# Kernel optimization log

Measured on AMD Instinct MI355X. Metric: run time of the kernel, lower is better.

Reference implementation:

```python
import jax, jax.numpy as jnp
import numpy as np

TOP_K = 2
EPS = 0.1
NUM_TOKENS = 524288
NUM_EXPERTS = 64
NEG_INF = -jnp.inf


def setup_inputs() -> dict:
    key = jax.random.key(0)
    router_logits = jax.random.normal(key, (NUM_TOKENS, NUM_EXPERTS), dtype=jnp.float32)
    return {"router_logits": router_logits}


def reference(router_logits):
    logits = router_logits.astype(jnp.float32)
    n = logits.shape[0]
    rows = jnp.arange(n)
    idx_list = []
    val_list = []
    for i in range(TOP_K):
        if i > 0:
            # mask out the previous maximum (argmax of current logits)
            prev = jnp.argmax(logits, axis=-1)
            logits = logits.at[rows, prev].set(NEG_INF)
        max_values = jnp.max(logits, axis=-1, keepdims=True)      # [n,1]
        max_indices = jnp.argmax(logits, axis=-1)                 # [n]
        # sparse-mixer mask: entries too far below the max get -inf
        denom = jnp.maximum(jnp.abs(logits), max_values)
        mask = (max_values - logits) / denom > 2.0 * EPS          # NaN at -inf entries -> False, kept -inf by logits value
        masked_logits = jnp.where(mask, NEG_INF, logits)
        sm = jax.nn.softmax(masked_logits, axis=-1)
        sel = jnp.take_along_axis(sm, max_indices[:, None], axis=-1)[:, 0]
        idx_list.append(max_indices)
        val_list.append(sel)
    topk_indices = jnp.stack(idx_list, axis=1).astype(jnp.int32)  # [n, top_k]
    topk_values = jnp.stack(val_list, axis=1)                     # [n, top_k]
    return topk_indices, topk_values
```

## Files before the change

### kernel.cpp

```cpp
#include <hip/hip_runtime.h>
#include <math.h>


#define SM_NEG_INF (-INFINITY)

__global__ __launch_bounds__(256) void sparse_mixer_routing_kernel(
    const float* __restrict__ logits, float* __restrict__ out, int n_tokens) {
  int tid = blockIdx.x * 256 + threadIdx.x;
  int token = tid >> 4;
  int sub = tid & 15;
  if (token >= n_tokens) return;

  const float4* rowp = (const float4*)(logits + (size_t)token * 64);
  float4 v = rowp[sub];
  float x[4] = {v.x, v.y, v.z, v.w};
  const int ebase = sub * 4;

  float m1 = x[0];
  int i1 = ebase;
#pragma unroll
  for (int j = 1; j < 4; ++j) {
    if (x[j] > m1) { m1 = x[j]; i1 = ebase + j; }
  }
#pragma unroll
  for (int d = 1; d < 16; d <<= 1) {
    float om = __shfl_xor(m1, d, 16);
    int   oi = __shfl_xor(i1, d, 16);
    if (om > m1 || (om == m1 && oi < i1)) { m1 = om; i1 = oi; }
  }

  float xe[4];
#pragma unroll
  for (int j = 0; j < 4; ++j) {
    xe[j] = ((ebase + j) == i1) ? SM_NEG_INF : x[j];
  }
  float m2 = xe[0];
  int i2 = ebase;
#pragma unroll
  for (int j = 1; j < 4; ++j) {
    if (xe[j] > m2) { m2 = xe[j]; i2 = ebase + j; }
  }
#pragma unroll
  for (int d = 1; d < 16; d <<= 1) {
    float om = __shfl_xor(m2, d, 16);
    int   oi = __shfl_xor(i2, d, 16);
    if (om > m2 || (om == m2 && oi < i2)) { m2 = om; i2 = oi; }
  }

  float s1 = 0.0f, s2 = 0.0f;
#pragma unroll
  for (int j = 0; j < 4; ++j) {
    {
      float xj = x[j];
      float a = m1 - xj;
      float den = fmaxf(fabsf(xj), m1);
      bool masked = (a / den) > 0.2f;
      float e = __expf(xj - m1);
      s1 += masked ? 0.0f : e;
    }
    {
      float xj = xe[j];
      float a = m2 - xj;
      float den = fmaxf(fabsf(xj), m2);
      bool masked = (a / den) > 0.2f;
      float e = __expf(xj - m2);
      s2 += masked ? 0.0f : e;
    }
  }
#pragma unroll
  for (int d = 1; d < 16; d <<= 1) {
    s1 += __shfl_xor(s1, d, 16);
    s2 += __shfl_xor(s2, d, 16);
  }

  if (sub == 0) {
    float v1 = 1.0f / s1;
    float v2 = 1.0f / s2;
    float2* idxp = (float2*)out + token;
    float2* valp = (float2*)(out + 2 * (size_t)n_tokens) + token;
    *idxp = make_float2((float)i1, (float)i2);
    *valp = make_float2(v1, v2);
  }
}

extern "C" void kernel_launch(void* const* d_in, const int* in_sizes, int n_in,
                              void* d_out, int out_size, void* d_ws, size_t ws_size,
                              hipStream_t stream) {
  const float* logits = (const float*)d_in[0];
  int n_tokens = in_sizes[0] / 64;
  float* out = (float*)d_out;

  int total_threads = n_tokens * 16;
  int block = 256;
  int grid = (total_threads + block - 1) / block;
  hipLaunchKernelGGL(sparse_mixer_routing_kernel, dim3(grid), dim3(block), 0,
                     stream, logits, out, n_tokens);
}
```

Baseline: 196.4 us.

## Use 8 lanes per token, share exp between passes, replace division mask

Each token is now handled by 8 lanes with two float4 loads each, halving shuffle stages and thread count. The mask test a/den > 0.2 becomes a double-precision multiply comparison against an exact threshold, so the fp32 divide goes away. One exp per element is computed relative to m1 and reused for the second softmax, which is corrected at the end by exp(m2-m1). Output stores are split across two lanes and use the hardware reciprocal. Double-precision compares add cost, and the rescaled exponent and fast reciprocal may differ slightly numerically.

```diff
diff --git a/kernel.cpp b/kernel.cpp
--- a/kernel.cpp
+++ b/kernel.cpp
@@ -2,84 +2,81 @@
 #include <math.h>
 
 
-#define SM_NEG_INF (-INFINITY)
-
 __global__ __launch_bounds__(256) void sparse_mixer_routing_kernel(
     const float* __restrict__ logits, float* __restrict__ out, int n_tokens) {
   int tid = blockIdx.x * 256 + threadIdx.x;
-  int token = tid >> 4;
-  int sub = tid & 15;
+  int token = tid >> 3;
+  int sub = tid & 7;
   if (token >= n_tokens) return;
 
-  const float4* rowp = (const float4*)(logits + (size_t)token * 64);
-  float4 v = rowp[sub];
-  float x[4] = {v.x, v.y, v.z, v.w};
-  const int ebase = sub * 4;
+  const float4* rowp = (const float4*)(logits + (size_t)token * 64) + sub * 2;
+  float4 va = rowp[0];
+  float4 vb = rowp[1];
+  float x[8] = {va.x, va.y, va.z, va.w, vb.x, vb.y, vb.z, vb.w};
+  const int ebase = sub * 8;
 
   float m1 = x[0];
   int i1 = ebase;
 #pragma unroll
-  for (int j = 1; j < 4; ++j) {
+  for (int j = 1; j < 8; ++j) {
     if (x[j] > m1) { m1 = x[j]; i1 = ebase + j; }
   }
 #pragma unroll
-  for (int d = 1; d < 16; d <<= 1) {
-    float om = __shfl_xor(m1, d, 16);
-    int   oi = __shfl_xor(i1, d, 16);
+  for (int d = 1; d < 8; d <<= 1) {
+    float om = __shfl_xor(m1, d, 8);
+    int   oi = __shfl_xor(i1, d, 8);
     if (om > m1 || (om == m1 && oi < i1)) { m1 = om; i1 = oi; }
   }
 
-  float xe[4];
-#pragma unroll
-  for (int j = 0; j < 4; ++j) {
-    xe[j] = ((ebase + j) == i1) ? SM_NEG_INF : x[j];
-  }
-  float m2 = xe[0];
+  float m2 = -INFINITY;
   int i2 = ebase;
 #pragma unroll
-  for (int j = 1; j < 4; ++j) {
-    if (xe[j] > m2) { m2 = xe[j]; i2 = ebase + j; }
+  for (int j = 0; j < 8; ++j) {
+    float xv = ((ebase + j) == i1) ? -INFINITY : x[j];
+    if (xv > m2) { m2 = xv; i2 = ebase + j; }
   }
 #pragma unroll
-  for (int d = 1; d < 16; d <<= 1) {
-    float om = __shfl_xor(m2, d, 16);
-    int   oi = __shfl_xor(i2, d, 16);
+  for (int d = 1; d < 8; d <<= 1) {
+    float om = __shfl_xor(m2, d, 8);
+    int   oi = __shfl_xor(i2, d, 8);
     if (om > m2 || (om == m2 && oi < i2)) { m2 = om; i2 = oi; }
   }
 
+  const double t_d = 26843547.0 / 134217728.0;
   float s1 = 0.0f, s2 = 0.0f;
 #pragma unroll
-  for (int j = 0; j < 4; ++j) {
-    {
-      float xj = x[j];
-      float a = m1 - xj;
-      float den = fmaxf(fabsf(xj), m1);
-      bool masked = (a / den) > 0.2f;
-      float e = __expf(xj - m1);
-      s1 += masked ? 0.0f : e;
-    }
-    {
-      float xj = xe[j];
-      float a = m2 - xj;
-      float den = fmaxf(fabsf(xj), m2);
-      bool masked = (a / den) > 0.2f;
-      float e = __expf(xj - m2);
-      s2 += masked ? 0.0f : e;
-    }
+  for (int j = 0; j < 8; ++j) {
+    float xj = x[j];
+    float a1 = m1 - xj;
+    float den1 = fmaxf(fabsf(xj), m1);
+    bool k1 = !((double)a1 > t_d * (double)den1);
+    float e = __expf(-a1);
+    s1 += k1 ? e : 0.0f;
+
+    float a2 = m2 - xj;
+    float den2 = fmaxf(fabsf(xj), m2);
+    bool k2 = !((double)a2 > t_d * (double)den2) && ((ebase + j) != i1);
+    s2 += k2 ? e : 0.0f;
   }
 #pragma unroll
-  for (int d = 1; d < 16; d <<= 1) {
-    s1 += __shfl_xor(s1, d, 16);
-    s2 += __shfl_xor(s2, d, 16);
+  for (int d = 1; d < 8; d <<= 1) {
+    s1 += __shfl_xor(s1, d, 8);
+    s2 += __shfl_xor(s2, d, 8);
   }
 
-  if (sub == 0) {
-    float v1 = 1.0f / s1;
-    float v2 = 1.0f / s2;
-    float2* idxp = (float2*)out + token;
-    float2* valp = (float2*)(out + 2 * (size_t)n_tokens) + token;
-    *idxp = make_float2((float)i1, (float)i2);
-    *valp = make_float2(v1, v2);
+  if (sub < 2) {
+    float2 r;
+    float2* dst;
+    if (sub == 0) {
+      r = make_float2((float)i1, (float)i2);
+      dst = (float2*)out + token;
+    } else {
+      float v1 = __builtin_amdgcn_rcpf(s1);
+      float v2 = __expf(m2 - m1) * __builtin_amdgcn_rcpf(s2);
+      r = make_float2(v1, v2);
+      dst = (float2*)(out + 2 * (size_t)n_tokens) + token;
+    }
+    *dst = r;
   }
 }
 
@@ -90,7 +87,7 @@
   int n_tokens = in_sizes[0] / 64;
   float* out = (float*)d_out;
 
-  int total_threads = n_tokens * 16;
+  int total_threads = n_tokens * 8;
   int block = 256;
   int grid = (total_threads + block - 1) / block;
   hipLaunchKernelGGL(sparse_mixer_routing_kernel, dim3(grid), dim3(block), 0,
```

Measured after the change: 187.5 us. -4.5%, faster.
